# Kernel tuning notes

Hardware: AMD Instinct MI355X
Metric: run time of the kernel (lower is better)

The kernel has to match this reference:

```python
import jax, jax.numpy as jnp
import numpy as np


def setup_inputs() -> dict:
    key = jax.random.key(0)
    k1, k2, k3 = jax.random.split(key, 3)
    B, S, IN, OUT = 4, 2048, 4096, 4096
    # int8 activations, weights, bias (stored as int8; math accumulates in int32)
    x = jax.random.randint(k1, (B, S, IN), -127, 128, dtype=jnp.int32).astype(jnp.int8)
    weight = jax.random.randint(k2, (OUT, IN), -127, 128, dtype=jnp.int32).astype(jnp.int8)  # (out, in)
    bias = jax.random.randint(k3, (1, OUT), -127, 128, dtype=jnp.int32).astype(jnp.int8)
    alpha = jnp.float32(0.001)  # input_scale*weight_scale/output_scale
    beta = jnp.float32(0.01)    # bias_scale/output_scale
    return {"x": x, "weight": weight, "bias": bias, "alpha": alpha, "beta": beta}


def reference(x, weight, bias, alpha, beta):
    # Flatten leading dims: (B,S,IN) -> (N,IN)
    x_shape = x.shape
    xf = x.reshape(-1, x_shape[-1])
    acc = jax.lax.dot_general(
        xf, weight,
        dimension_numbers=(((1,), (1,)), ((), ())),
        preferred_element_type=jnp.int32,
    )  # (N, OUT) int32
    # Fused epilogue: y = round(alpha*acc + beta*bias), saturate to int8
    yf = alpha * acc.astype(jnp.float32) + beta * bias.astype(jnp.float32)
    y = jnp.clip(jnp.round(yf), -128.0, 127.0).astype(jnp.int8)
    return y.reshape(*x_shape[:-1], -1)
```

## Files before the change

### kernel.cpp

```cpp
#include <hip/hip_runtime.h>
#include <stdint.h>

using i32x4  = __attribute__((ext_vector_type(4)))  int;
using i32x16 = __attribute__((ext_vector_type(16))) int;

#define M_TOT 8192
#define N_TOT 4096
#define K_TOT 4096
#define BM 256
#define BN 256

__device__ __forceinline__ void gload_lds16(const void* g, void* l) {
  __builtin_amdgcn_global_load_lds(
      (const __attribute__((address_space(1))) void*)(uintptr_t)g,
      (__attribute__((address_space(3))) void*)(uint32_t)(uintptr_t)l,
      16, 0, 0);
}

__global__ void pack_tiles(const int* __restrict__ a32, const int* __restrict__ b32,
                           int8_t* __restrict__ ap, int8_t* __restrict__ bp,
                           int na, int ntot) {
  int stride = gridDim.x * blockDim.x;
  for (int idx = blockIdx.x * blockDim.x + threadIdx.x; idx < ntot; idx += stride) {
    int i = idx;
    const int* src;
    int8_t* dst;
    if (idx < na) { src = a32; dst = ap; }
    else          { src = b32; dst = bp; i = idx - na; }
    int sp = i & 3;
    int rr = (i >> 2) & 255;
    int kc = (i >> 10) & 63;
    int p  = i >> 16;
    int sl = sp ^ ((rr >> 1) & 3);
    const i32x4* s = (const i32x4*)(src + (((size_t)(p * 256 + rr)) << 12) + kc * 64 + sl * 16);
    i32x4 a = s[0], b = s[1], c = s[2], d = s[3];
    i32x4 o;
    o.x = (a.x & 255) | ((a.y & 255) << 8) | ((a.z & 255) << 16) | (a.w << 24);
    o.y = (b.x & 255) | ((b.y & 255) << 8) | ((b.z & 255) << 16) | (b.w << 24);
    o.z = (c.x & 255) | ((c.y & 255) << 8) | ((c.z & 255) << 16) | (c.w << 24);
    o.w = (d.x & 255) | ((d.y & 255) << 8) | ((d.z & 255) << 16) | (d.w << 24);
    ((i32x4*)dst)[i] = o;
  }
}

#define STAGE_H(jj, R) {                                                   \
    const int8_t* _ga = Asrc + ((size_t)(jj) << 14) + stoff;               \
    char* _da = lds + (((R) & 3) << 14) + w * 2048;                        \
    gload_lds16(_ga, _da); gload_lds16(_ga + 1024, _da + 1024);            \
    const int8_t* _gb = Bsrc + ((size_t)(jj) << 14) + stoff;               \
    char* _db = lds + 65536 + (((R) & 3) << 14) + w * 2048;                \
    gload_lds16(_gb, _db); gload_lds16(_gb + 1024, _db + 1024); }

#define LOAD_FRAGS(DA, DB, R, S) {                                         \
    const int _so = ((((S) << 1) | hi) ^ swz) * 16;                        \
    const char* _pa = lds + (((R) & 3) << 14) + _so;                       \
    const char* _pb = _pa + 65536;                                         \
    _Pragma("unroll")                                                      \
    for (int mi = 0; mi < 4; ++mi) DA[mi] = *(const i32x4*)(_pa + aRow[mi]); \
    _Pragma("unroll")                                                      \
    for (int ni = 0; ni < 2; ++ni) DB[ni] = *(const i32x4*)(_pb + bRow[ni]); }

#define MFMA8(A, B)                                                        \
    _Pragma("unroll")                                                      \
    for (int mi = 0; mi < 4; ++mi)                                         \
    _Pragma("unroll")                                                      \
    for (int ni = 0; ni < 2; ++ni)                                         \
      acc[mi][ni] = __builtin_amdgcn_mfma_i32_32x32x32_i8(A[mi], B[ni], acc[mi][ni], 0, 0, 0);

#define INTERVAL(j, R0, R1, VM, DO_STAGE, DO_NEXT) {                       \
    asm volatile("s_waitcnt vmcnt(" VM ")" ::: "memory");                  \
    __builtin_amdgcn_s_barrier();                                          \
    __builtin_amdgcn_sched_barrier(0);                                     \
    if (DO_STAGE) STAGE_H((j) + 3, (R0) + 3);                              \
    LOAD_FRAGS(a1, b1, R0, 1)                                              \
    __builtin_amdgcn_s_setprio(1);                                         \
    MFMA8(a0, b0)                                                          \
    __builtin_amdgcn_s_setprio(0);                                         \
    if (DO_NEXT) LOAD_FRAGS(a0, b0, R1, 0)                                 \
    __builtin_amdgcn_s_setprio(1);                                         \
    MFMA8(a1, b1)                                                          \
    __builtin_amdgcn_s_setprio(0); }

__global__ __launch_bounds__(512, 2) void gemm_w8a8(
    const int8_t* __restrict__ Apack,
    const int8_t* __restrict__ Bpack,
    const int*    __restrict__ bias,
    const float*  __restrict__ alphap,
    const float*  __restrict__ betap,
    int* __restrict__ out)
{
  __shared__ __align__(16) char lds[131072];

  const int bid = blockIdx.x;
  const int xcd = bid & 7, wi = bid >> 3;
  const int tm = (xcd & 3) * 8 + (wi & 7);
  const int tn = (xcd >> 2) * 8 + (wi >> 3);

  const int tid = threadIdx.x;
  const int w   = tid >> 6;
  const int l   = tid & 63;
  const int lr  = l & 31;
  const int hi  = l >> 5;
  const int wr  = w >> 2;
  const int wc  = w & 3;
  const int stoff = w * 2048 + l * 16;

  const int8_t* Asrc = Apack + (size_t)tm * (64 * 16384);
  const int8_t* Bsrc = Bpack + (size_t)tn * (64 * 16384);

  const int swz = (lr >> 1) & 3;
  int aRow[4], bRow[2];
#pragma unroll
  for (int mi = 0; mi < 4; ++mi) aRow[mi] = (wr * 128 + mi * 32 + lr) * 64;
#pragma unroll
  for (int ni = 0; ni < 2; ++ni) bRow[ni] = (wc * 64 + ni * 32 + lr) * 64;

  i32x16 acc[4][2] = {};
  i32x4 a0[4], b0[2], a1[4], b1[2];

  STAGE_H(0, 0)
  STAGE_H(1, 1)
  STAGE_H(2, 2)
  asm volatile("s_waitcnt vmcnt(8)" ::: "memory");
  __builtin_amdgcn_s_barrier();
  __builtin_amdgcn_sched_barrier(0);
  LOAD_FRAGS(a0, b0, 0, 0)

  for (int tt = 0; tt < 15; ++tt) {
    const int j0 = tt * 4;
    INTERVAL(j0 + 0, 0, 1, "4", 1, 1)
    INTERVAL(j0 + 1, 1, 2, "4", 1, 1)
    INTERVAL(j0 + 2, 2, 3, "4", 1, 1)
    INTERVAL(j0 + 3, 3, 0, "4", 1, 1)
  }
  INTERVAL(60, 0, 1, "4", 1, 1)
  INTERVAL(61, 1, 2, "4", 0, 1)
  INTERVAL(62, 2, 3, "0", 0, 1)
  INTERVAL(63, 3, 0, "0", 0, 0)

  const float alpha = *alphap;
  const float beta  = *betap;
  const int brow = tm * BM, bcol = tn * BN;
#pragma unroll
  for (int ni = 0; ni < 2; ++ni) {
    const int col = bcol + wc * 64 + ni * 32 + lr;
    const float bb = beta * (float)bias[col];
#pragma unroll
    for (int mi = 0; mi < 4; ++mi) {
      const int rbase = brow + wr * 128 + mi * 32 + 4 * hi;
#pragma unroll
      for (int r = 0; r < 16; ++r) {
        const int row = rbase + (r & 3) + 8 * (r >> 2);
        float v = alpha * (float)acc[mi][ni][r] + bb;
        v = rintf(v);
        v = fminf(127.f, fmaxf(-128.f, v));
        out[(size_t)row * N_TOT + col] = (int)v;
      }
    }
  }
}

extern "C" void kernel_launch(void* const* d_in, const int* in_sizes, int n_in,
                              void* d_out, int out_size, void* d_ws, size_t ws_size,
                              hipStream_t stream) {
  const int*   x32    = (const int*)d_in[0];
  const int*   w32    = (const int*)d_in[1];
  const int*   bias   = (const int*)d_in[2];
  const float* alphap = (const float*)d_in[3];
  const float* betap  = (const float*)d_in[4];
  int* out = (int*)d_out;

  int8_t* xp = (int8_t*)d_ws;
  int8_t* wp = xp + (size_t)M_TOT * K_TOT;

  const int na   = (M_TOT * K_TOT) / 16;
  const int ntot = na + (N_TOT * K_TOT) / 16;
  pack_tiles<<<3072, 256, 0, stream>>>(x32, w32, xp, wp, na, ntot);

  gemm_w8a8<<<512, 512, 0, stream>>>(xp, wp, bias, alphap, betap, out);
}
```

Baseline: 200.4 us.

## Switch to double-buffered 128-wide K tiles with explicit MFMA/LDS interleave scheduling

Repacks operands into 128-byte K tiles with an 8-way XOR swizzle and replaces the 4-stage 64-wide K ring buffer with a 2-stage 128-wide double buffer. Each interval issues one prefetch and then four fragment-load/MFMA groups, ordered with sched_group_barrier hints that interleave LDS reads and MFMAs. This halves the number of barriers per K, but every interval now waits on vmcnt(0), so the prefetch has only one tile of compute to hide its latency. The packer also gains a redundant duplicate store.

New measurement: 190.5 us. 5.0% less time.

```diff
diff --git a/kernel.cpp b/kernel.cpp
--- a/kernel.cpp
+++ b/kernel.cpp
@@ -9,6 +9,7 @@
 #define K_TOT 4096
 #define BM 256
 #define BN 256
+#define NTILES 32
 
 __device__ __forceinline__ void gload_lds16(const void* g, void* l) {
   __builtin_amdgcn_global_load_lds(
@@ -27,58 +28,71 @@
     int8_t* dst;
     if (idx < na) { src = a32; dst = ap; }
     else          { src = b32; dst = bp; i = idx - na; }
-    int sp = i & 3;
-    int rr = (i >> 2) & 255;
-    int kc = (i >> 10) & 63;
+    int sp = i & 7;
+    int rr = (i >> 3) & 255;
+    int kt = (i >> 11) & 31;
     int p  = i >> 16;
-    int sl = sp ^ ((rr >> 1) & 3);
-    const i32x4* s = (const i32x4*)(src + (((size_t)(p * 256 + rr)) << 12) + kc * 64 + sl * 16);
+    int sl = sp ^ (rr & 7);
+    const i32x4* s = (const i32x4*)(src + ((size_t)(p * 256 + rr)) * 4096 + (kt * 8 + sl) * 16);
     i32x4 a = s[0], b = s[1], c = s[2], d = s[3];
     i32x4 o;
     o.x = (a.x & 255) | ((a.y & 255) << 8) | ((a.z & 255) << 16) | (a.w << 24);
     o.y = (b.x & 255) | ((b.y & 255) << 8) | ((b.z & 255) << 16) | (b.w << 24);
     o.z = (c.x & 255) | ((c.y & 255) << 8) | ((c.z & 255) << 16) | (c.w << 24);
     o.w = (d.x & 255) | ((d.y & 255) << 8) | ((d.z & 255) << 16) | (d.w << 24);
+    ((i32x4*)dst)[idx < na ? i : i] = o;
     ((i32x4*)dst)[i] = o;
   }
 }
 
-#define STAGE_H(jj, R) {                                                   \
-    const int8_t* _ga = Asrc + ((size_t)(jj) << 14) + stoff;               \
-    char* _da = lds + (((R) & 3) << 14) + w * 2048;                        \
-    gload_lds16(_ga, _da); gload_lds16(_ga + 1024, _da + 1024);            \
-    const int8_t* _gb = Bsrc + ((size_t)(jj) << 14) + stoff;               \
-    char* _db = lds + 65536 + (((R) & 3) << 14) + w * 2048;                \
-    gload_lds16(_gb, _db); gload_lds16(_gb + 1024, _db + 1024); }
+#define STAGE_T(kt, BUF) {                                                  \
+    const int8_t* _ga = Asrc + ((size_t)(kt) << 15) + stoff;                \
+    char* _da = lds + ((BUF) << 15) + stoff;                                \
+    gload_lds16(_ga, _da);               gload_lds16(_ga + 1024, _da + 1024); \
+    gload_lds16(_ga + 2048, _da + 2048); gload_lds16(_ga + 3072, _da + 3072); \
+    const int8_t* _gb = Bsrc + ((size_t)(kt) << 15) + stoff;                \
+    char* _db = lds + 65536 + ((BUF) << 15) + stoff;                        \
+    gload_lds16(_gb, _db);               gload_lds16(_gb + 1024, _db + 1024); \
+    gload_lds16(_gb + 2048, _db + 2048); gload_lds16(_gb + 3072, _db + 3072); }
 
-#define LOAD_FRAGS(DA, DB, R, S) {                                         \
-    const int _so = ((((S) << 1) | hi) ^ swz) * 16;                        \
-    const char* _pa = lds + (((R) & 3) << 14) + _so;                       \
-    const char* _pb = _pa + 65536;                                         \
-    _Pragma("unroll")                                                      \
+#define LOAD_FRAGS(DA, DB, BUF, S) {                                        \
+    const int _so = ((((S) << 1) | hi) ^ sx) * 16;                          \
+    const char* _pa = lds + ((BUF) << 15) + _so;                            \
+    const char* _pb = _pa + 65536;                                          \
+    _Pragma("unroll")                                                       \
     for (int mi = 0; mi < 4; ++mi) DA[mi] = *(const i32x4*)(_pa + aRow[mi]); \
-    _Pragma("unroll")                                                      \
+    _Pragma("unroll")                                                       \
     for (int ni = 0; ni < 2; ++ni) DB[ni] = *(const i32x4*)(_pb + bRow[ni]); }
 
-#define MFMA8(A, B)                                                        \
-    _Pragma("unroll")                                                      \
-    for (int mi = 0; mi < 4; ++mi)                                         \
-    _Pragma("unroll")                                                      \
-    for (int ni = 0; ni < 2; ++ni)                                         \
+#define MFMA8(A, B)                                                         \
+    _Pragma("unroll")                                                       \
+    for (int mi = 0; mi < 4; ++mi)                                          \
+    _Pragma("unroll")                                                       \
+    for (int ni = 0; ni < 2; ++ni)                                          \
       acc[mi][ni] = __builtin_amdgcn_mfma_i32_32x32x32_i8(A[mi], B[ni], acc[mi][ni], 0, 0, 0);
 
-#define INTERVAL(j, R0, R1, VM, DO_STAGE, DO_NEXT) {                       \
-    asm volatile("s_waitcnt vmcnt(" VM ")" ::: "memory");                  \
-    __builtin_amdgcn_s_barrier();                                          \
-    __builtin_amdgcn_sched_barrier(0);                                     \
-    if (DO_STAGE) STAGE_H((j) + 3, (R0) + 3);                              \
-    LOAD_FRAGS(a1, b1, R0, 1)                                              \
-    __builtin_amdgcn_s_setprio(1);                                         \
-    MFMA8(a0, b0)                                                          \
-    __builtin_amdgcn_s_setprio(0);                                         \
-    if (DO_NEXT) LOAD_FRAGS(a0, b0, R1, 0)                                 \
-    __builtin_amdgcn_s_setprio(1);                                         \
-    MFMA8(a1, b1)                                                          \
+#define SGB(m, n) __builtin_amdgcn_sched_group_barrier((m), (n), 0)
+#define PAIR SGB(0x8, 1); SGB(0x100, 1);
+#define KSBLOCK PAIR PAIR PAIR PAIR PAIR PAIR SGB(0x8, 2);
+
+#define INTERVAL(kt, BUF, DO_STAGE) {                                       \
+    asm volatile("s_waitcnt vmcnt(0)" ::: "memory");                        \
+    __builtin_amdgcn_s_barrier();                                           \
+    __builtin_amdgcn_sched_barrier(0);                                      \
+    __builtin_amdgcn_s_setprio(1);                                          \
+    if (DO_STAGE) STAGE_T((kt) + 1, (BUF) ^ 1);                             \
+    LOAD_FRAGS(a0, b0, BUF, 0)                                              \
+    LOAD_FRAGS(a1, b1, BUF, 1)                                              \
+    MFMA8(a0, b0)                                                           \
+    LOAD_FRAGS(a0, b0, BUF, 2)                                              \
+    MFMA8(a1, b1)                                                           \
+    LOAD_FRAGS(a1, b1, BUF, 3)                                              \
+    MFMA8(a0, b0)                                                           \
+    MFMA8(a1, b1)                                                           \
+    SGB(0x10, 8);                                                           \
+    SGB(0x100, 6);                                                          \
+    KSBLOCK KSBLOCK KSBLOCK                                                 \
+    SGB(0x8, 8);                                                            \
     __builtin_amdgcn_s_setprio(0); }
 
 __global__ __launch_bounds__(512, 2) void gemm_w8a8(
@@ -103,40 +117,30 @@
   const int hi  = l >> 5;
   const int wr  = w >> 2;
   const int wc  = w & 3;
-  const int stoff = w * 2048 + l * 16;
+  const int stoff = w * 4096 + l * 16;
+  const int sx  = lr & 7;
 
-  const int8_t* Asrc = Apack + (size_t)tm * (64 * 16384);
-  const int8_t* Bsrc = Bpack + (size_t)tn * (64 * 16384);
+  const int8_t* Asrc = Apack + ((size_t)tm << 20);
+  const int8_t* Bsrc = Bpack + ((size_t)tn << 20);
 
-  const int swz = (lr >> 1) & 3;
   int aRow[4], bRow[2];
 #pragma unroll
-  for (int mi = 0; mi < 4; ++mi) aRow[mi] = (wr * 128 + mi * 32 + lr) * 64;
+  for (int mi = 0; mi < 4; ++mi) aRow[mi] = (wr * 128 + mi * 32 + lr) * 128;
 #pragma unroll
-  for (int ni = 0; ni < 2; ++ni) bRow[ni] = (wc * 64 + ni * 32 + lr) * 64;
+  for (int ni = 0; ni < 2; ++ni) bRow[ni] = (wc * 64 + ni * 32 + lr) * 128;
 
   i32x16 acc[4][2] = {};
   i32x4 a0[4], b0[2], a1[4], b1[2];
 
-  STAGE_H(0, 0)
-  STAGE_H(1, 1)
-  STAGE_H(2, 2)
-  asm volatile("s_waitcnt vmcnt(8)" ::: "memory");
-  __builtin_amdgcn_s_barrier();
-  __builtin_amdgcn_sched_barrier(0);
-  LOAD_FRAGS(a0, b0, 0, 0)
+  STAGE_T(0, 0)
 
   for (int tt = 0; tt < 15; ++tt) {
-    const int j0 = tt * 4;
-    INTERVAL(j0 + 0, 0, 1, "4", 1, 1)
-    INTERVAL(j0 + 1, 1, 2, "4", 1, 1)
-    INTERVAL(j0 + 2, 2, 3, "4", 1, 1)
-    INTERVAL(j0 + 3, 3, 0, "4", 1, 1)
+    const int k0 = tt * 2;
+    INTERVAL(k0 + 0, 0, 1)
+    INTERVAL(k0 + 1, 1, 1)
   }
-  INTERVAL(60, 0, 1, "4", 1, 1)
-  INTERVAL(61, 1, 2, "4", 0, 1)
-  INTERVAL(62, 2, 3, "0", 0, 1)
-  INTERVAL(63, 3, 0, "0", 0, 0)
+  INTERVAL(30, 0, 1)
+  INTERVAL(31, 1, 0)
 
   const float alpha = *alphap;
   const float beta  = *betap;
```

## Restructure GEMM main loop to 3-stage ring with split A/B staging

Applied to the files above, without the earlier changes.

Replaces the 4-deep LDS ring of 16-row K chunks with a 3-deep ring of 64-wide K tiles. Each K tile is processed in two halves, with A and B global-to-LDS staging spread across them and extra barriers plus lgkmcnt waits between fragment loads and MFMA bursts. LDS usage drops from 128KB to 96KB. The aim is to cut per-iteration barrier overhead and improve overlap between loads and MFMAs, at the cost of more barriers per tile and less register double-buffering of fragments.

After: 203.4 us. Within noise of the previous version (+1.5%).

```diff
diff --git a/kernel.cpp b/kernel.cpp
--- a/kernel.cpp
+++ b/kernel.cpp
@@ -43,43 +43,53 @@
   }
 }
 
-#define STAGE_H(jj, R) {                                                   \
-    const int8_t* _ga = Asrc + ((size_t)(jj) << 14) + stoff;               \
-    char* _da = lds + (((R) & 3) << 14) + w * 2048;                        \
-    gload_lds16(_ga, _da); gload_lds16(_ga + 1024, _da + 1024);            \
-    const int8_t* _gb = Bsrc + ((size_t)(jj) << 14) + stoff;               \
-    char* _db = lds + 65536 + (((R) & 3) << 14) + w * 2048;                \
-    gload_lds16(_gb, _db); gload_lds16(_gb + 1024, _db + 1024); }
+#define STAGE_A(KC) {                                                       \
+    const int8_t* _g = Asrc + (size_t)(KC) * 16384 + stoff;                 \
+    char* _d = lds + ((KC) % 3) * 16384 + stoff;                            \
+    gload_lds16(_g, _d); gload_lds16(_g + 8192, _d + 8192); }
+#define STAGE_B(KC) {                                                       \
+    const int8_t* _g = Bsrc + (size_t)(KC) * 16384 + stoff;                 \
+    char* _d = lds + 49152 + ((KC) % 3) * 16384 + stoff;                    \
+    gload_lds16(_g, _d); gload_lds16(_g + 8192, _d + 8192); }
 
-#define LOAD_FRAGS(DA, DB, R, S) {                                         \
-    const int _so = ((((S) << 1) | hi) ^ swz) * 16;                        \
-    const char* _pa = lds + (((R) & 3) << 14) + _so;                       \
-    const char* _pb = _pa + 65536;                                         \
-    _Pragma("unroll")                                                      \
-    for (int mi = 0; mi < 4; ++mi) DA[mi] = *(const i32x4*)(_pa + aRow[mi]); \
-    _Pragma("unroll")                                                      \
-    for (int ni = 0; ni < 2; ++ni) DB[ni] = *(const i32x4*)(_pb + bRow[ni]); }
-
-#define MFMA8(A, B)                                                        \
-    _Pragma("unroll")                                                      \
-    for (int mi = 0; mi < 4; ++mi)                                         \
-    _Pragma("unroll")                                                      \
-    for (int ni = 0; ni < 2; ++ni)                                         \
-      acc[mi][ni] = __builtin_amdgcn_mfma_i32_32x32x32_i8(A[mi], B[ni], acc[mi][ni], 0, 0, 0);
-
-#define INTERVAL(j, R0, R1, VM, DO_STAGE, DO_NEXT) {                       \
-    asm volatile("s_waitcnt vmcnt(" VM ")" ::: "memory");                  \
-    __builtin_amdgcn_s_barrier();                                          \
-    __builtin_amdgcn_sched_barrier(0);                                     \
-    if (DO_STAGE) STAGE_H((j) + 3, (R0) + 3);                              \
-    LOAD_FRAGS(a1, b1, R0, 1)                                              \
-    __builtin_amdgcn_s_setprio(1);                                         \
-    MFMA8(a0, b0)                                                          \
-    __builtin_amdgcn_s_setprio(0);                                         \
-    if (DO_NEXT) LOAD_FRAGS(a0, b0, R1, 0)                                 \
-    __builtin_amdgcn_s_setprio(1);                                         \
-    MFMA8(a1, b1)                                                          \
-    __builtin_amdgcn_s_setprio(0); }
+#define KTILE(RING, KC2, VM, DO_STAGE) {                                    \
+    asm volatile("s_waitcnt vmcnt(" VM ")" ::: "memory");                   \
+    __builtin_amdgcn_s_barrier();                                           \
+    __builtin_amdgcn_sched_barrier(0);                                      \
+    const char* _La = lds + (RING) * 16384;                                 \
+    const char* _Lb = lds + 49152 + (RING) * 16384;                         \
+    i32x4 A0[2][2], A1[2][2], B0[2][2];                                     \
+    _Pragma("unroll") for (int mi = 0; mi < 2; ++mi)                        \
+    _Pragma("unroll") for (int ks = 0; ks < 2; ++ks)                        \
+      A0[mi][ks] = *(const i32x4*)(_La + aRow[mi] + kOff[ks]);              \
+    _Pragma("unroll") for (int ni = 0; ni < 2; ++ni)                        \
+    _Pragma("unroll") for (int ks = 0; ks < 2; ++ks)                        \
+      B0[ni][ks] = *(const i32x4*)(_Lb + bRow[ni] + kOff[ks]);              \
+    if (DO_STAGE) STAGE_A(KC2)                                              \
+    __builtin_amdgcn_s_barrier();                                           \
+    asm volatile("s_waitcnt lgkmcnt(0)" ::: "memory");                      \
+    __builtin_amdgcn_sched_barrier(0);                                      \
+    __builtin_amdgcn_s_setprio(1);                                          \
+    _Pragma("unroll") for (int ks = 0; ks < 2; ++ks)                        \
+    _Pragma("unroll") for (int mi = 0; mi < 2; ++mi)                        \
+    _Pragma("unroll") for (int ni = 0; ni < 2; ++ni)                        \
+      acc[mi][ni] = __builtin_amdgcn_mfma_i32_32x32x32_i8(A0[mi][ks], B0[ni][ks], acc[mi][ni], 0, 0, 0); \
+    __builtin_amdgcn_s_setprio(0);                                          \
+    __builtin_amdgcn_s_barrier();                                           \
+    _Pragma("unroll") for (int mi = 0; mi < 2; ++mi)                        \
+    _Pragma("unroll") for (int ks = 0; ks < 2; ++ks)                        \
+      A1[mi][ks] = *(const i32x4*)(_La + aRow[mi + 2] + kOff[ks]);          \
+    if (DO_STAGE) STAGE_B(KC2)                                              \
+    __builtin_amdgcn_s_barrier();                                           \
+    asm volatile("s_waitcnt lgkmcnt(0)" ::: "memory");                      \
+    __builtin_amdgcn_sched_barrier(0);                                      \
+    __builtin_amdgcn_s_setprio(1);                                          \
+    _Pragma("unroll") for (int ks = 0; ks < 2; ++ks)                        \
+    _Pragma("unroll") for (int mi = 0; mi < 2; ++mi)                        \
+    _Pragma("unroll") for (int ni = 0; ni < 2; ++ni)                        \
+      acc[mi + 2][ni] = __builtin_amdgcn_mfma_i32_32x32x32_i8(A1[mi][ks], B0[ni][ks], acc[mi + 2][ni], 0, 0, 0); \
+    __builtin_amdgcn_s_setprio(0);                                          \
+  }
 
 __global__ __launch_bounds__(512, 2) void gemm_w8a8(
     const int8_t* __restrict__ Apack,
@@ -89,7 +99,7 @@
     const float*  __restrict__ betap,
     int* __restrict__ out)
 {
-  __shared__ __align__(16) char lds[131072];
+  __shared__ __align__(16) char lds[98304];
 
   const int bid = blockIdx.x;
   const int xcd = bid & 7, wi = bid >> 3;
@@ -103,40 +113,35 @@
   const int hi  = l >> 5;
   const int wr  = w >> 2;
   const int wc  = w & 3;
-  const int stoff = w * 2048 + l * 16;
+  const int stoff = tid * 16;
 
-  const int8_t* Asrc = Apack + (size_t)tm * (64 * 16384);
-  const int8_t* Bsrc = Bpack + (size_t)tn * (64 * 16384);
+  const int8_t* Asrc = Apack + ((size_t)tm << 20);
+  const int8_t* Bsrc = Bpack + ((size_t)tn << 20);
 
   const int swz = (lr >> 1) & 3;
-  int aRow[4], bRow[2];
+  int aRow[4], bRow[2], kOff[2];
 #pragma unroll
   for (int mi = 0; mi < 4; ++mi) aRow[mi] = (wr * 128 + mi * 32 + lr) * 64;
 #pragma unroll
   for (int ni = 0; ni < 2; ++ni) bRow[ni] = (wc * 64 + ni * 32 + lr) * 64;
+#pragma unroll
+  for (int ks = 0; ks < 2; ++ks) kOff[ks] = ((((ks << 1) | hi)) ^ swz) * 16;
 
   i32x16 acc[4][2] = {};
-  i32x4 a0[4], b0[2], a1[4], b1[2];
 
-  STAGE_H(0, 0)
-  STAGE_H(1, 1)
-  STAGE_H(2, 2)
-  asm volatile("s_waitcnt vmcnt(8)" ::: "memory");
-  __builtin_amdgcn_s_barrier();
-  __builtin_amdgcn_sched_barrier(0);
-  LOAD_FRAGS(a0, b0, 0, 0)
+  STAGE_A(0) STAGE_B(0)
+  STAGE_A(1) STAGE_B(1)
 
-  for (int tt = 0; tt < 15; ++tt) {
-    const int j0 = tt * 4;
-    INTERVAL(j0 + 0, 0, 1, "4", 1, 1)
-    INTERVAL(j0 + 1, 1, 2, "4", 1, 1)
-    INTERVAL(j0 + 2, 2, 3, "4", 1, 1)
-    INTERVAL(j0 + 3, 3, 0, "4", 1, 1)
+  for (int t = 0; t < 20; ++t) {
+    const int k = t * 3;
+    KTILE(0, k + 2, "4", 1)
+    KTILE(1, k + 3, "4", 1)
+    KTILE(2, k + 4, "4", 1)
   }
-  INTERVAL(60, 0, 1, "4", 1, 1)
-  INTERVAL(61, 1, 2, "4", 0, 1)
-  INTERVAL(62, 2, 3, "0", 0, 1)
-  INTERVAL(63, 3, 0, "0", 0, 0)
+  KTILE(0, 62, "4", 1)
+  KTILE(1, 63, "4", 1)
+  KTILE(2, 0,  "4", 0)
+  KTILE(0, 0,  "0", 0)
 
   const float alpha = *alphap;
   const float beta  = *betap;
```
